# Kernel optimization log

Hardware: AMD Instinct MI355X
Metric: run time of the kernel (lower is better)

The kernel has to match this reference:

```python
import jax, jax.numpy as jnp
import numpy as np

L = 2048      # seq_len
E = 2048      # hidden_dim
H = 16        # num_heads
D = E // H    # head_dim


def setup_inputs() -> dict:
    key = jax.random.key(0)
    ks = jax.random.split(key, 6)
    x = jax.random.normal(ks[0], (L, E), dtype=jnp.float32)
    bias_matrix = jax.random.normal(ks[1], (L, L), dtype=jnp.float32) * 0.1
    # nn.MultiheadAttention params: packed in_proj [3E, E] + bias [3E], out_proj [E, E] + bias [E]
    in_proj_weight = jax.random.normal(ks[2], (3 * E, E), dtype=jnp.float32) * 0.02
    in_proj_bias = jax.random.normal(ks[3], (3 * E,), dtype=jnp.float32) * 0.02
    out_proj_weight = jax.random.normal(ks[4], (E, E), dtype=jnp.float32) * 0.02
    out_proj_bias = jax.random.normal(ks[5], (E,), dtype=jnp.float32) * 0.02
    return {
        "x": x,
        "bias_matrix": bias_matrix,
        "in_proj_weight": in_proj_weight,
        "in_proj_bias": in_proj_bias,
        "out_proj_weight": out_proj_weight,
        "out_proj_bias": out_proj_bias,
    }


def reference(x, bias_matrix, in_proj_weight, in_proj_bias, out_proj_weight, out_proj_bias):
    # Packed QKV projection (torch Linear convention: y = x @ W.T + b)
    qkv = x @ in_proj_weight.T + in_proj_bias            # [L, 3E]
    q, k, v = jnp.split(qkv, 3, axis=-1)                 # each [L, E]
    q = q.reshape(L, H, D)
    k = k.reshape(L, H, D)
    v = v.reshape(L, H, D)
    scale = 1.0 / jnp.sqrt(jnp.asarray(D, dtype=x.dtype))
    # scores: [H, L, L]; bias_matrix broadcast over heads (torch 2D attn_mask semantics)
    scores = jnp.einsum("lhd,mhd->hlm", q * scale, k) + bias_matrix[None, :, :]
    attn = jax.nn.softmax(scores, axis=-1)
    ctx = jnp.einsum("hlm,mhd->lhd", attn, v).reshape(L, E)
    out = ctx @ out_proj_weight.T + out_proj_bias        # [L, E]
    return out
```

## Files before the change

kernel.cpp:

```cpp
#include <hip/hip_runtime.h>
#include <math.h>

#define L_SEQ 2048
#define E_DIM 2048
#define H_NUM 16
#define D_HEAD 128

typedef __attribute__((ext_vector_type(8))) _Float16 half8;
typedef __attribute__((ext_vector_type(4))) _Float16 half4;
typedef __attribute__((ext_vector_type(4))) float floatx4;

static __device__ __forceinline__ void gload16(const void* g, void* lds) {
  __builtin_amdgcn_global_load_lds(
      (const __attribute__((address_space(1))) void*)g,
      (__attribute__((address_space(3))) void*)lds, 16, 0, 0);
}

__global__ __launch_bounds__(256)
void cvt3_f32_f16(const float* __restrict__ a, _Float16* __restrict__ oa, int na,
                  const float* __restrict__ b, _Float16* __restrict__ ob, int nb,
                  const float* __restrict__ c, _Float16* __restrict__ oc, int nc) {
  int i = (blockIdx.x * 256 + threadIdx.x) * 8;
  const float* src;
  _Float16* dst;
  if (i < na) {
    src = a + i; dst = oa + i;
  } else if (i < na + nb) {
    src = b + (i - na); dst = ob + (i - na);
  } else if (i < na + nb + nc) {
    src = c + (i - na - nb); dst = oc + (i - na - nb);
  } else {
    return;
  }
  float4 p = *(const float4*)src;
  float4 q = *(const float4*)(src + 4);
  half8 h = {(_Float16)p.x, (_Float16)p.y, (_Float16)p.z, (_Float16)p.w,
             (_Float16)q.x, (_Float16)q.y, (_Float16)q.z, (_Float16)q.w};
  *(half8*)dst = h;
}

template <int TM, int TN, int WR, int WC, int EPI>
__global__ __launch_bounds__(256)
void gemm_mfma(const _Float16* __restrict__ A, const _Float16* __restrict__ B,
               const float* __restrict__ bias, float* __restrict__ C,
               _Float16* __restrict__ qk, _Float16* __restrict__ vt,
               int M, int N, int K) {
  constexpr int RT = TM / (16 * WR);
  constexpr int CT = TN / (16 * WC);
  constexpr int ACH = TM / 8;
  constexpr int NCH = (TM + TN) / 32;

  __shared__ _Float16 As[2][TM * 64];
  __shared__ _Float16 Bs[2][TN * 64];

  const int tid = threadIdx.x;
  const int wave = tid >> 6, lane = tid & 63;
  const int l15 = lane & 15, quad = lane >> 4;
  const int wr = wave / WC, wc = wave % WC;
  const int row0 = blockIdx.y * TM, col0 = blockIdx.x * TN;

  const int srow = lane >> 3;
  const int gc = (lane & 7) ^ srow;

  auto stage = [&](int buf, int k0) {
#pragma unroll
    for (int c = 0; c < NCH; ++c) {
      int chunk = wave * NCH + c;
      if (chunk < ACH) {
        int row = chunk * 8 + srow;
        gload16((const char*)(A + (size_t)(row0 + row) * K + k0) + gc * 16,
                (char*)&As[buf][0] + chunk * 1024);
      } else {
        int bch = chunk - ACH;
        int row = bch * 8 + srow;
        gload16((const char*)(B + (size_t)(col0 + row) * K + k0) + gc * 16,
                (char*)&Bs[buf][0] + bch * 1024);
      }
    }
  };

  floatx4 acc[RT][CT];
#pragma unroll
  for (int i = 0; i < RT; ++i)
#pragma unroll
    for (int j = 0; j < CT; ++j) acc[i][j] = (floatx4){0.f, 0.f, 0.f, 0.f};

  const int niter = K / 64;
  stage(0, 0);

  for (int it = 0; it < niter; ++it) {
    const int cur = it & 1;
    __syncthreads();
    if (it + 1 < niter) stage(cur ^ 1, (it + 1) * 64);

#pragma unroll
    for (int ks = 0; ks < 2; ++ks) {
      half8 af[RT], bf[CT];
#pragma unroll
      for (int t = 0; t < RT; ++t) {
        int r = wr * (16 * RT) + t * 16 + l15;
        af[t] = *(const half8*)&As[cur][r * 64 + (((ks * 4 + quad) ^ (r & 7)) * 8)];
      }
#pragma unroll
      for (int t = 0; t < CT; ++t) {
        int r = wc * (16 * CT) + t * 16 + l15;
        bf[t] = *(const half8*)&Bs[cur][r * 64 + (((ks * 4 + quad) ^ (r & 7)) * 8)];
      }
#pragma unroll
      for (int tr = 0; tr < RT; ++tr)
#pragma unroll
        for (int tc = 0; tc < CT; ++tc)
          acc[tr][tc] = __builtin_amdgcn_mfma_f32_16x16x32_f16(
              af[tr], bf[tc], acc[tr][tc], 0, 0, 0);
    }
  }

  const int crow = row0 + wr * (16 * RT);
  const int ccol = col0 + wc * (16 * CT);

  if (EPI == 0) {
#pragma unroll
    for (int tc = 0; tc < CT; ++tc) {
      int col = ccol + tc * 16 + l15;
      float bb = bias[col];
#pragma unroll
      for (int tr = 0; tr < RT; ++tr)
#pragma unroll
        for (int r = 0; r < 4; ++r)
          C[(size_t)(crow + tr * 16 + quad * 4 + r) * N + col] =
              acc[tr][tc][r] + bb;
    }
  } else if (col0 < 2 * E_DIM) {
#pragma unroll
    for (int tc = 0; tc < CT; ++tc) {
      int col = ccol + tc * 16 + l15;
      float bb = bias[col];
#pragma unroll
      for (int tr = 0; tr < RT; ++tr)
#pragma unroll
        for (int r = 0; r < 4; ++r)
          qk[(size_t)(crow + tr * 16 + quad * 4 + r) * (2 * E_DIM) + col] =
              (_Float16)(acc[tr][tc][r] + bb);
    }
  } else {
#pragma unroll
    for (int tc = 0; tc < CT; ++tc) {
      int col = ccol + tc * 16 + l15;
      float bb = bias[col];
      int vrow = col - 2 * E_DIM;
#pragma unroll
      for (int tr = 0; tr < RT; ++tr) {
        int rbase = crow + tr * 16 + quad * 4;
        half4 h = {(_Float16)(acc[tr][tc][0] + bb), (_Float16)(acc[tr][tc][1] + bb),
                   (_Float16)(acc[tr][tc][2] + bb), (_Float16)(acc[tr][tc][3] + bb)};
        *(half4*)&vt[(size_t)vrow * L_SEQ + rbase] = h;
      }
    }
  }
}

__global__ __launch_bounds__(512, 2)
void attn_mfma(const _Float16* __restrict__ qk, const _Float16* __restrict__ vt,
               const float* __restrict__ bias, _Float16* __restrict__ ctx) {
  const int h = blockIdx.x;
  const int q0 = blockIdx.y * 128;
  const int tid = threadIdx.x;
  const int wave = tid >> 6;
  const int lane = tid & 63;
  const int l15 = lane & 15;
  const int quad = lane >> 4;

  __shared__ _Float16 Ks[2][64][136];
  __shared__ _Float16 Vst[2][128][72];
  __shared__ _Float16 Ps[128][72];

  half8 qa[4];
  {
    const _Float16* qp = qk + (size_t)(q0 + wave * 16 + l15) * (2 * E_DIM) +
                         h * D_HEAD + quad * 8;
#pragma unroll
    for (int ks = 0; ks < 4; ++ks) qa[ks] = *(const half8*)(qp + ks * 32);
  }

  float l_i = 0.f;
  floatx4 o[8];
#pragma unroll
  for (int t = 0; t < 8; ++t) o[t] = (floatx4){0.f, 0.f, 0.f, 0.f};

  const float scale = 0.088388347648318447f;

  half8 kreg[2], vreg[2];
  floatx4 bcur[4], bnxt[4];
#pragma unroll
  for (int c = 0; c < 2; ++c) {
    int m = c * 512 + tid;
    kreg[c] = *(const half8*)(qk + (size_t)(m >> 4) * (2 * E_DIM) + E_DIM +
                              h * D_HEAD + (m & 15) * 8);
    vreg[c] = *(const half8*)(vt + (size_t)(h * D_HEAD + (m >> 3)) * L_SEQ +
                              (m & 7) * 8);
  }
#pragma unroll
  for (int t = 0; t < 4; ++t)
    bcur[t] = *(const floatx4*)&bias[(size_t)(q0 + wave * 16 + l15) * L_SEQ +
                                    16 * t + quad * 4];
#pragma unroll
  for (int c = 0; c < 2; ++c) {
    int m = c * 512 + tid;
    *(half8*)&Ks[0][m >> 4][(m & 15) * 8] = kreg[c];
    *(half8*)&Vst[0][m >> 3][(m & 7) * 8] = vreg[c];
  }

#pragma unroll 2
  for (int it = 0; it < 32; ++it) {
    const int cur = it & 1, nxt = cur ^ 1;
    const int kt = it * 64;
    __syncthreads();

    if (it < 31) {
#pragma unroll
      for (int c = 0; c < 2; ++c) {
        int m = c * 512 + tid;
        kreg[c] = *(const half8*)(qk + (size_t)(kt + 64 + (m >> 4)) * (2 * E_DIM) +
                                  E_DIM + h * D_HEAD + (m & 15) * 8);
        vreg[c] = *(const half8*)(vt + (size_t)(h * D_HEAD + (m >> 3)) * L_SEQ +
                                  kt + 64 + (m & 7) * 8);
      }
#pragma unroll
      for (int t = 0; t < 4; ++t)
        bnxt[t] = *(const floatx4*)&bias[(size_t)(q0 + wave * 16 + l15) * L_SEQ +
                                         kt + 64 + 16 * t + quad * 4];
    }

    floatx4 st[4];
#pragma unroll
    for (int t = 0; t < 4; ++t) st[t] = (floatx4){0.f, 0.f, 0.f, 0.f};
#pragma unroll
    for (int ks = 0; ks < 4; ++ks)
#pragma unroll
      for (int t = 0; t < 4; ++t) {
        half8 kf = *(const half8*)&Ks[cur][16 * t + l15][ks * 32 + quad * 8];
        st[t] = __builtin_amdgcn_mfma_f32_16x16x32_f16(kf, qa[ks], st[t], 0, 0, 0);
      }

    {
      float ls = 0.f;
      float ps[4][4];
#pragma unroll
      for (int t = 0; t < 4; ++t)
#pragma unroll
        for (int r = 0; r < 4; ++r) {
          float p = __expf(fmaf(st[t][r], scale, bcur[t][r]));
          ps[t][r] = p;
          ls += p;
        }
      ls += __shfl_xor(ls, 16);
      ls += __shfl_xor(ls, 32);
      l_i += ls;
#pragma unroll
      for (int t = 0; t < 4; ++t) {
        half4 hp = {(_Float16)ps[t][0], (_Float16)ps[t][1],
                    (_Float16)ps[t][2], (_Float16)ps[t][3]};
        *(half4*)&Ps[wave * 16 + l15][16 * t + quad * 4] = hp;
      }
    }

    half8 pa[2];
#pragma unroll
    for (int ks = 0; ks < 2; ++ks)
      pa[ks] = *(const half8*)&Ps[wave * 16 + l15][ks * 32 + quad * 8];
#pragma unroll
    for (int t = 0; t < 8; ++t)
#pragma unroll
      for (int ks = 0; ks < 2; ++ks) {
        half8 vf = *(const half8*)&Vst[cur][16 * t + l15][ks * 32 + quad * 8];
        o[t] = __builtin_amdgcn_mfma_f32_16x16x32_f16(pa[ks], vf, o[t], 0, 0, 0);
      }

    if (it < 31) {
#pragma unroll
      for (int c = 0; c < 2; ++c) {
        int m = c * 512 + tid;
        *(half8*)&Ks[nxt][m >> 4][(m & 15) * 8] = kreg[c];
        *(half8*)&Vst[nxt][m >> 3][(m & 7) * 8] = vreg[c];
      }
#pragma unroll
      for (int t = 0; t < 4; ++t) bcur[t] = bnxt[t];
    }
  }

  float inv[4];
#pragma unroll
  for (int r = 0; r < 4; ++r) inv[r] = 1.f / __shfl(l_i, quad * 4 + r);
#pragma unroll
  for (int t = 0; t < 8; ++t)
#pragma unroll
    for (int r = 0; r < 4; ++r) {
      int row = q0 + wave * 16 + quad * 4 + r;
      ctx[(size_t)row * E_DIM + h * D_HEAD + 16 * t + l15] =
          (_Float16)(o[t][r] * inv[r]);
    }
}

extern "C" void kernel_launch(void* const* d_in, const int* in_sizes, int n_in,
                              void* d_out, int out_size, void* d_ws, size_t ws_size,
                              hipStream_t stream) {
  const float* x          = (const float*)d_in[0];
  const float* bias_mat   = (const float*)d_in[1];
  const float* in_proj_w  = (const float*)d_in[2];
  const float* in_proj_b  = (const float*)d_in[3];
  const float* out_proj_w = (const float*)d_in[4];
  const float* out_proj_b = (const float*)d_in[5];
  float* out = (float*)d_out;

  _Float16* x16 = (_Float16*)d_ws;
  _Float16* w1  = x16 + (size_t)L_SEQ * E_DIM;
  _Float16* w2  = w1 + (size_t)3 * E_DIM * E_DIM;
  _Float16* qk  = w2 + (size_t)E_DIM * E_DIM;
  _Float16* vt  = qk + (size_t)L_SEQ * 2 * E_DIM;
  _Float16* ctx = vt + (size_t)E_DIM * L_SEQ;

  dim3 blk(256);
  const int nx = L_SEQ * E_DIM, nw1 = 3 * E_DIM * E_DIM, nw2 = E_DIM * E_DIM;

  cvt3_f32_f16<<<(nx + nw1 + nw2) / 2048, blk, 0, stream>>>(
      x, x16, nx, in_proj_w, w1, nw1, out_proj_w, w2, nw2);

  gemm_mfma<128, 128, 2, 2, 1><<<dim3(3 * E_DIM / 128, L_SEQ / 128), blk, 0, stream>>>(
      x16, w1, in_proj_b, nullptr, qk, vt, L_SEQ, 3 * E_DIM, E_DIM);

  attn_mfma<<<dim3(H_NUM, L_SEQ / 128), dim3(512), 0, stream>>>(qk, vt, bias_mat,
                                                                ctx);

  gemm_mfma<128, 64, 4, 1, 0><<<dim3(E_DIM / 64, L_SEQ / 128), blk, 0, stream>>>(
      ctx, w2, out_proj_b, out, nullptr, nullptr, L_SEQ, E_DIM, E_DIM);
}
```

Baseline: 279.6 us.

## Restructure attention kernel with split-KV wave pairs, async LDS loads, register-resident P

Waves are paired so that each wave handles 32 query rows against its own 64-key half of a 128-key stage. The two partial outputs and row sums are merged through LDS at the end. K/V tiles are fetched straight into swizzled LDS with global_load_lds, replacing the register round-trip and padding. The P matrix stays in registers and feeds 16x16x16 MFMAs directly, which drops the Ps LDS write and read, and each K fragment is now reused for two Q subtiles. The cost is 128KB of LDS per block and more registers, which may limit occupancy below the 2-block launch bound.

```diff
diff --git a/kernel.cpp b/kernel.cpp
--- a/kernel.cpp
+++ b/kernel.cpp
@@ -169,136 +169,164 @@
   const int lane = tid & 63;
   const int l15 = lane & 15;
   const int quad = lane >> 4;
-
-  __shared__ _Float16 Ks[2][64][136];
-  __shared__ _Float16 Vst[2][128][72];
-  __shared__ _Float16 Ps[128][72];
-
-  half8 qa[4];
-  {
-    const _Float16* qp = qk + (size_t)(q0 + wave * 16 + l15) * (2 * E_DIM) +
-                         h * D_HEAD + quad * 8;
-#pragma unroll
-    for (int ks = 0; ks < 4; ++ks) qa[ks] = *(const half8*)(qp + ks * 32);
-  }
-
-  float l_i = 0.f;
-  floatx4 o[8];
-#pragma unroll
-  for (int t = 0; t < 8; ++t) o[t] = (floatx4){0.f, 0.f, 0.f, 0.f};
+  const int g = wave >> 1;
+  const int p = wave & 1;
+
+  __shared__ __align__(16) char smem[131072];
+  char* const ksmem = smem;
+  char* const vsmem = smem + 65536;
+
+  const int qrow = q0 + g * 32;
+
+  half8 qa[2][4];
+#pragma unroll
+  for (int u = 0; u < 2; ++u) {
+    const _Float16* qp =
+        qk + (size_t)(qrow + u * 16 + l15) * (2 * E_DIM) + h * D_HEAD + quad * 8;
+#pragma unroll
+    for (int ks = 0; ks < 4; ++ks) qa[u][ks] = *(const half8*)(qp + ks * 32);
+  }
+
+  float l_acc[2] = {0.f, 0.f};
+  floatx4 o[2][8];
+#pragma unroll
+  for (int u = 0; u < 2; ++u)
+#pragma unroll
+    for (int t = 0; t < 8; ++t) o[u][t] = (floatx4){0.f, 0.f, 0.f, 0.f};
 
   const float scale = 0.088388347648318447f;
 
-  half8 kreg[2], vreg[2];
-  floatx4 bcur[4], bnxt[4];
-#pragma unroll
-  for (int c = 0; c < 2; ++c) {
-    int m = c * 512 + tid;
-    kreg[c] = *(const half8*)(qk + (size_t)(m >> 4) * (2 * E_DIM) + E_DIM +
-                              h * D_HEAD + (m & 15) * 8);
-    vreg[c] = *(const half8*)(vt + (size_t)(h * D_HEAD + (m >> 3)) * L_SEQ +
-                              (m & 7) * 8);
-  }
-#pragma unroll
-  for (int t = 0; t < 4; ++t)
-    bcur[t] = *(const floatx4*)&bias[(size_t)(q0 + wave * 16 + l15) * L_SEQ +
-                                    16 * t + quad * 4];
-#pragma unroll
-  for (int c = 0; c < 2; ++c) {
-    int m = c * 512 + tid;
-    *(half8*)&Ks[0][m >> 4][(m & 15) * 8] = kreg[c];
-    *(half8*)&Vst[0][m >> 3][(m & 7) * 8] = vreg[c];
-  }
+  auto stage_pair = [&](int kt2, int sb) {
+#pragma unroll
+    for (int c = 0; c < 8; ++c) {
+      int mb = c * 512 + (tid & ~63);
+      int m = mb + (tid & 63);
+      if (mb < 2048) {
+        int sub = mb >> 10;
+        int idx = m & 1023, idx0 = mb & 1023;
+        int row = idx >> 4, cc = idx & 15;
+        gload16(qk + (size_t)(kt2 + sub * 64 + row) * (2 * E_DIM) + E_DIM +
+                    h * D_HEAD + ((cc ^ (row & 7)) * 8),
+                ksmem + (sb + sub) * 16384 + idx0 * 16);
+      } else {
+        int mm = mb - 2048;
+        int sub = mm >> 10;
+        int idx = (m - 2048) & 1023, idx0 = mm & 1023;
+        int row = idx >> 3, cc = idx & 7;
+        gload16(vt + (size_t)(h * D_HEAD + row) * L_SEQ + kt2 + sub * 64 +
+                    ((cc ^ (row & 7)) * 8),
+                vsmem + (sb + sub) * 16384 + idx0 * 16);
+      }
+    }
+  };
+
+  stage_pair(0, 0);
 
 #pragma unroll 2
-  for (int it = 0; it < 32; ++it) {
-    const int cur = it & 1, nxt = cur ^ 1;
-    const int kt = it * 64;
+  for (int s = 0; s < 16; ++s) {
+    const int kt = s * 128 + p * 64;
+    const int slot = (s & 1) * 2 + p;
     __syncthreads();
 
-    if (it < 31) {
-#pragma unroll
-      for (int c = 0; c < 2; ++c) {
-        int m = c * 512 + tid;
-        kreg[c] = *(const half8*)(qk + (size_t)(kt + 64 + (m >> 4)) * (2 * E_DIM) +
-                                  E_DIM + h * D_HEAD + (m & 15) * 8);
-        vreg[c] = *(const half8*)(vt + (size_t)(h * D_HEAD + (m >> 3)) * L_SEQ +
-                                  kt + 64 + (m & 7) * 8);
-      }
-#pragma unroll
-      for (int t = 0; t < 4; ++t)
-        bnxt[t] = *(const floatx4*)&bias[(size_t)(q0 + wave * 16 + l15) * L_SEQ +
-                                         kt + 64 + 16 * t + quad * 4];
-    }
-
-    floatx4 st[4];
-#pragma unroll
-    for (int t = 0; t < 4; ++t) st[t] = (floatx4){0.f, 0.f, 0.f, 0.f};
+    floatx4 bq[2][4];
+#pragma unroll
+    for (int u = 0; u < 2; ++u)
+#pragma unroll
+      for (int t4 = 0; t4 < 4; ++t4)
+        bq[u][t4] = *(const floatx4*)&bias[(size_t)(qrow + u * 16 + l15) * L_SEQ +
+                                           kt + t4 * 16 + quad * 4];
+
+    if (s < 15) stage_pair((s + 1) * 128, ((s + 1) & 1) * 2);
+
+    const char* ksb = ksmem + slot * 16384;
+    floatx4 st[2][4];
+#pragma unroll
+    for (int u = 0; u < 2; ++u)
+#pragma unroll
+      for (int t4 = 0; t4 < 4; ++t4) st[u][t4] = (floatx4){0.f, 0.f, 0.f, 0.f};
 #pragma unroll
     for (int ks = 0; ks < 4; ++ks)
 #pragma unroll
-      for (int t = 0; t < 4; ++t) {
-        half8 kf = *(const half8*)&Ks[cur][16 * t + l15][ks * 32 + quad * 8];
-        st[t] = __builtin_amdgcn_mfma_f32_16x16x32_f16(kf, qa[ks], st[t], 0, 0, 0);
-      }
-
-    {
+      for (int t4 = 0; t4 < 4; ++t4) {
+        int row = t4 * 16 + l15;
+        half8 kf = *(const half8*)(ksb + row * 256 +
+                                   (((4 * ks + quad) ^ (row & 7)) * 16));
+        st[0][t4] = __builtin_amdgcn_mfma_f32_16x16x32_f16(kf, qa[0][ks],
+                                                           st[0][t4], 0, 0, 0);
+        st[1][t4] = __builtin_amdgcn_mfma_f32_16x16x32_f16(kf, qa[1][ks],
+                                                           st[1][t4], 0, 0, 0);
+      }
+
+    half4 hp[2][4];
+#pragma unroll
+    for (int u = 0; u < 2; ++u) {
       float ls = 0.f;
-      float ps[4][4];
-#pragma unroll
-      for (int t = 0; t < 4; ++t)
-#pragma unroll
-        for (int r = 0; r < 4; ++r) {
-          float p = __expf(fmaf(st[t][r], scale, bcur[t][r]));
-          ps[t][r] = p;
-          ls += p;
-        }
+#pragma unroll
+      for (int t4 = 0; t4 < 4; ++t4) {
+        float p0 = __expf(fmaf(st[u][t4][0], scale, bq[u][t4][0]));
+        float p1 = __expf(fmaf(st[u][t4][1], scale, bq[u][t4][1]));
+        float p2 = __expf(fmaf(st[u][t4][2], scale, bq[u][t4][2]));
+        float p3 = __expf(fmaf(st[u][t4][3], scale, bq[u][t4][3]));
+        ls += (p0 + p1) + (p2 + p3);
+        hp[u][t4] = (half4){(_Float16)p0, (_Float16)p1, (_Float16)p2, (_Float16)p3};
+      }
       ls += __shfl_xor(ls, 16);
       ls += __shfl_xor(ls, 32);
-      l_i += ls;
-#pragma unroll
-      for (int t = 0; t < 4; ++t) {
-        half4 hp = {(_Float16)ps[t][0], (_Float16)ps[t][1],
-                    (_Float16)ps[t][2], (_Float16)ps[t][3]};
-        *(half4*)&Ps[wave * 16 + l15][16 * t + quad * 4] = hp;
-      }
-    }
-
-    half8 pa[2];
-#pragma unroll
-    for (int ks = 0; ks < 2; ++ks)
-      pa[ks] = *(const half8*)&Ps[wave * 16 + l15][ks * 32 + quad * 8];
-#pragma unroll
-    for (int t = 0; t < 8; ++t)
-#pragma unroll
-      for (int ks = 0; ks < 2; ++ks) {
-        half8 vf = *(const half8*)&Vst[cur][16 * t + l15][ks * 32 + quad * 8];
-        o[t] = __builtin_amdgcn_mfma_f32_16x16x32_f16(pa[ks], vf, o[t], 0, 0, 0);
-      }
-
-    if (it < 31) {
-#pragma unroll
-      for (int c = 0; c < 2; ++c) {
-        int m = c * 512 + tid;
-        *(half8*)&Ks[nxt][m >> 4][(m & 15) * 8] = kreg[c];
-        *(half8*)&Vst[nxt][m >> 3][(m & 7) * 8] = vreg[c];
-      }
-#pragma unroll
-      for (int t = 0; t < 4; ++t) bcur[t] = bnxt[t];
-    }
-  }
-
-  float inv[4];
-#pragma unroll
-  for (int r = 0; r < 4; ++r) inv[r] = 1.f / __shfl(l_i, quad * 4 + r);
-#pragma unroll
-  for (int t = 0; t < 8; ++t)
-#pragma unroll
-    for (int r = 0; r < 4; ++r) {
-      int row = q0 + wave * 16 + quad * 4 + r;
-      ctx[(size_t)row * E_DIM + h * D_HEAD + 16 * t + l15] =
-          (_Float16)(o[t][r] * inv[r]);
-    }
+      l_acc[u] += ls;
+    }
+
+    const char* vsb = vsmem + slot * 16384;
+#pragma unroll
+    for (int tk = 0; tk < 4; ++tk)
+#pragma unroll
+      for (int td = 0; td < 8; ++td) {
+        int row = td * 16 + l15;
+        half4 vf = *(const half4*)(vsb + row * 128 +
+                                   (((2 * tk + (quad >> 1)) ^ (row & 7)) * 16) +
+                                   (quad & 1) * 8);
+        o[0][td] = __builtin_amdgcn_mfma_f32_16x16x16f16(hp[0][tk], vf,
+                                                         o[0][td], 0, 0, 0);
+        o[1][td] = __builtin_amdgcn_mfma_f32_16x16x16f16(hp[1][tk], vf,
+                                                         o[1][td], 0, 0, 0);
+      }
+  }
+
+  float* obuf = (float*)smem;
+  float* lbuf = (float*)(smem + 73728);
+  __syncthreads();
+  if (p == 1) {
+#pragma unroll
+    for (int u = 0; u < 2; ++u)
+#pragma unroll
+      for (int t = 0; t < 8; ++t)
+        *(floatx4*)&obuf[(size_t)(g * 128 + t * 16 + l15) * 36 + u * 16 + quad * 4] =
+            o[u][t];
+    if (quad == 0) {
+      lbuf[(g * 2 + 0) * 16 + l15] = l_acc[0];
+      lbuf[(g * 2 + 1) * 16 + l15] = l_acc[1];
+    }
+  }
+  __syncthreads();
+  if (p == 0) {
+#pragma unroll
+    for (int u = 0; u < 2; ++u) {
+      float lt = l_acc[u] + lbuf[(g * 2 + u) * 16 + l15];
+      float inv[4];
+#pragma unroll
+      for (int r = 0; r < 4; ++r) inv[r] = 1.f / __shfl(lt, quad * 4 + r);
+#pragma unroll
+      for (int t = 0; t < 8; ++t) {
+        floatx4 part = *(const floatx4*)&obuf[(size_t)(g * 128 + t * 16 + l15) * 36 +
+                                              u * 16 + quad * 4];
+#pragma unroll
+        for (int r = 0; r < 4; ++r) {
+          int rowq = qrow + u * 16 + quad * 4 + r;
+          ctx[(size_t)rowq * E_DIM + h * D_HEAD + t * 16 + l15] =
+              (_Float16)((o[u][t][r] + part[r]) * inv[r]);
+        }
+      }
+    }
+  }
 }
 
 extern "C" void kernel_launch(void* const* d_in, const int* in_sizes, int n_in,
```

Result: no change. 282.7 us (+1.1%).

## Add dedicated 256x256-tile QKV GEMM kernel with deeper LDS pipelining

Applied to the files above, without the earlier changes.

Replaces the generic 128x128 QKV projection GEMM with a specialized kernel using 512 threads, 256x256 output tiles and 128 KB of LDS. K is split into half-tiles staged through a multi-slot buffer with explicit vmcnt waits, so global-to-LDS loads overlap MFMA compute. The larger tile raises arithmetic intensity per LDS byte, at the cost of one block per CU and only 192 blocks, which may leave some CUs idle. The generic GEMM template loses its QKV epilogue and keeps only the fp32 output path.

```diff
diff --git a/kernel.cpp b/kernel.cpp
--- a/kernel.cpp
+++ b/kernel.cpp
@@ -39,11 +39,130 @@
   *(half8*)dst = h;
 }
 
-template <int TM, int TN, int WR, int WC, int EPI>
+__global__ __launch_bounds__(512, 1)
+void gemm_qkv(const _Float16* __restrict__ A, const _Float16* __restrict__ B,
+              const float* __restrict__ bias, _Float16* __restrict__ qk,
+              _Float16* __restrict__ vt) {
+  constexpr int K = E_DIM;
+  __shared__ __align__(16) char smem[131072];
+  char* const Asm = smem;
+  char* const Bsm = smem + 65536;
+
+  const int tid = threadIdx.x;
+  const int wave = tid >> 6, lane = tid & 63;
+  const int l15 = lane & 15, quad = lane >> 4;
+  const int wm = wave >> 2, wn = wave & 3;
+  const int brow = blockIdx.y * 256, bcol = blockIdx.x * 256;
+
+  const _Float16* Ag = A + (size_t)brow * K;
+  const _Float16* Bg = B + (size_t)bcol * K;
+
+  auto stg = [&](char* smbase, const _Float16* gbase, int T, int kh) {
+    char* slot = smbase + ((T & 1) * 2 + kh) * 16384;
+#pragma unroll
+    for (int j = 0; j < 2; ++j) {
+      int mb = j * 512 + (tid & ~63);
+      int m = mb + (tid & 63);
+      int row = m >> 2, c = m & 3;
+      gload16(gbase + (size_t)row * K + T * 64 + kh * 32 + ((c ^ (row & 3)) * 8),
+              slot + mb * 16);
+    }
+  };
+
+  floatx4 acc[8][4];
+#pragma unroll
+  for (int i = 0; i < 8; ++i)
+#pragma unroll
+    for (int j = 0; j < 4; ++j) acc[i][j] = (floatx4){0.f, 0.f, 0.f, 0.f};
+
+  auto compute_phase = [&](int T, int ks) {
+    const char* Ab = Asm + ((T & 1) * 2 + ks) * 16384;
+    const char* Bb = Bsm + ((T & 1) * 2 + ks) * 16384;
+    half8 af[8], bf[4];
+#pragma unroll
+    for (int t = 0; t < 8; ++t)
+      af[t] = *(const half8*)(Ab + (size_t)(wm * 128 + t * 16 + l15) * 64 +
+                              ((quad ^ (l15 & 3)) * 16));
+#pragma unroll
+    for (int t = 0; t < 4; ++t)
+      bf[t] = *(const half8*)(Bb + (size_t)(wn * 64 + t * 16 + l15) * 64 +
+                              ((quad ^ (l15 & 3)) * 16));
+#pragma unroll
+    for (int i = 0; i < 8; ++i)
+#pragma unroll
+      for (int j = 0; j < 4; ++j)
+        acc[i][j] = __builtin_amdgcn_mfma_f32_16x16x32_f16(af[i], bf[j],
+                                                           acc[i][j], 0, 0, 0);
+  };
+
+  stg(Asm, Ag, 0, 0); stg(Bsm, Bg, 0, 0);
+  stg(Asm, Ag, 0, 1); stg(Bsm, Bg, 0, 1);
+  stg(Asm, Ag, 1, 0); stg(Bsm, Bg, 1, 0);
+
+  for (int T = 0; T < 31; ++T) {
+    __builtin_amdgcn_sched_barrier(0);
+    asm volatile("s_waitcnt vmcnt(8) lgkmcnt(0)" ::: "memory");
+    __builtin_amdgcn_s_barrier();
+    __builtin_amdgcn_sched_barrier(0);
+    stg(Asm, Ag, T + 1, 1);
+    stg(Bsm, Bg, T + 1, 1);
+    compute_phase(T, 0);
+    __builtin_amdgcn_sched_barrier(0);
+    asm volatile("s_waitcnt vmcnt(8) lgkmcnt(0)" ::: "memory");
+    __builtin_amdgcn_s_barrier();
+    __builtin_amdgcn_sched_barrier(0);
+    if (T < 30) {
+      stg(Asm, Ag, T + 2, 0);
+      stg(Bsm, Bg, T + 2, 0);
+    }
+    compute_phase(T, 1);
+  }
+  __builtin_amdgcn_sched_barrier(0);
+  asm volatile("s_waitcnt vmcnt(4) lgkmcnt(0)" ::: "memory");
+  __builtin_amdgcn_s_barrier();
+  __builtin_amdgcn_sched_barrier(0);
+  compute_phase(31, 0);
+  __builtin_amdgcn_sched_barrier(0);
+  asm volatile("s_waitcnt vmcnt(0) lgkmcnt(0)" ::: "memory");
+  __builtin_amdgcn_s_barrier();
+  __builtin_amdgcn_sched_barrier(0);
+  compute_phase(31, 1);
+
+  const int crow = brow + wm * 128;
+  const int ccol0 = bcol + wn * 64;
+  if (bcol < 2 * E_DIM) {
+#pragma unroll
+    for (int j = 0; j < 4; ++j) {
+      int col = ccol0 + j * 16 + l15;
+      float bb = bias[col];
+#pragma unroll
+      for (int i = 0; i < 8; ++i)
+#pragma unroll
+        for (int r = 0; r < 4; ++r)
+          qk[(size_t)(crow + i * 16 + quad * 4 + r) * (2 * E_DIM) + col] =
+              (_Float16)(acc[i][j][r] + bb);
+    }
+  } else {
+#pragma unroll
+    for (int j = 0; j < 4; ++j) {
+      int col = ccol0 + j * 16 + l15;
+      float bb = bias[col];
+      int vrow = col - 2 * E_DIM;
+#pragma unroll
+      for (int i = 0; i < 8; ++i) {
+        int rbase = crow + i * 16 + quad * 4;
+        half4 h = {(_Float16)(acc[i][j][0] + bb), (_Float16)(acc[i][j][1] + bb),
+                   (_Float16)(acc[i][j][2] + bb), (_Float16)(acc[i][j][3] + bb)};
+        *(half4*)&vt[(size_t)vrow * L_SEQ + rbase] = h;
+      }
+    }
+  }
+}
+
+template <int TM, int TN, int WR, int WC>
 __global__ __launch_bounds__(256)
 void gemm_mfma(const _Float16* __restrict__ A, const _Float16* __restrict__ B,
                const float* __restrict__ bias, float* __restrict__ C,
-               _Float16* __restrict__ qk, _Float16* __restrict__ vt,
                int M, int N, int K) {
   constexpr int RT = TM / (16 * WR);
   constexpr int CT = TN / (16 * WC);
@@ -118,44 +237,16 @@
   const int crow = row0 + wr * (16 * RT);
   const int ccol = col0 + wc * (16 * CT);
 
-  if (EPI == 0) {
-#pragma unroll
-    for (int tc = 0; tc < CT; ++tc) {
-      int col = ccol + tc * 16 + l15;
-      float bb = bias[col];
-#pragma unroll
-      for (int tr = 0; tr < RT; ++tr)
-#pragma unroll
-        for (int r = 0; r < 4; ++r)
-          C[(size_t)(crow + tr * 16 + quad * 4 + r) * N + col] =
-              acc[tr][tc][r] + bb;
-    }
-  } else if (col0 < 2 * E_DIM) {
-#pragma unroll
-    for (int tc = 0; tc < CT; ++tc) {
-      int col = ccol + tc * 16 + l15;
-      float bb = bias[col];
-#pragma unroll
-      for (int tr = 0; tr < RT; ++tr)
-#pragma unroll
-        for (int r = 0; r < 4; ++r)
-          qk[(size_t)(crow + tr * 16 + quad * 4 + r) * (2 * E_DIM) + col] =
-              (_Float16)(acc[tr][tc][r] + bb);
-    }
-  } else {
-#pragma unroll
-    for (int tc = 0; tc < CT; ++tc) {
-      int col = ccol + tc * 16 + l15;
-      float bb = bias[col];
-      int vrow = col - 2 * E_DIM;
-#pragma unroll
-      for (int tr = 0; tr < RT; ++tr) {
-        int rbase = crow + tr * 16 + quad * 4;
-        half4 h = {(_Float16)(acc[tr][tc][0] + bb), (_Float16)(acc[tr][tc][1] + bb),
-                   (_Float16)(acc[tr][tc][2] + bb), (_Float16)(acc[tr][tc][3] + bb)};
-        *(half4*)&vt[(size_t)vrow * L_SEQ + rbase] = h;
-      }
-    }
+#pragma unroll
+  for (int tc = 0; tc < CT; ++tc) {
+    int col = ccol + tc * 16 + l15;
+    float bb = bias[col];
+#pragma unroll
+    for (int tr = 0; tr < RT; ++tr)
+#pragma unroll
+      for (int r = 0; r < 4; ++r)
+        C[(size_t)(crow + tr * 16 + quad * 4 + r) * N + col] =
+            acc[tr][tc][r] + bb;
   }
 }
 
@@ -325,12 +416,12 @@
   cvt3_f32_f16<<<(nx + nw1 + nw2) / 2048, blk, 0, stream>>>(
       x, x16, nx, in_proj_w, w1, nw1, out_proj_w, w2, nw2);
 
-  gemm_mfma<128, 128, 2, 2, 1><<<dim3(3 * E_DIM / 128, L_SEQ / 128), blk, 0, stream>>>(
-      x16, w1, in_proj_b, nullptr, qk, vt, L_SEQ, 3 * E_DIM, E_DIM);
+  gemm_qkv<<<dim3(3 * E_DIM / 256, L_SEQ / 256), dim3(512), 0, stream>>>(
+      x16, w1, in_proj_b, qk, vt);
 
   attn_mfma<<<dim3(H_NUM, L_SEQ / 128), dim3(512), 0, stream>>>(qk, vt, bias_mat,
                                                                 ctx);
 
-  gemm_mfma<128, 64, 4, 1, 0><<<dim3(E_DIM / 64, L_SEQ / 128), blk, 0, stream>>>(
-      ctx, w2, out_proj_b, out, nullptr, nullptr, L_SEQ, E_DIM, E_DIM);
-}
+  gemm_mfma<128, 64, 4, 1><<<dim3(E_DIM / 64, L_SEQ / 128), blk, 0, stream>>>(
+      ctx, w2, out_proj_b, out, L_SEQ, E_DIM, E_DIM);
+}
```

After: 281.2 us. Within noise of the previous version (+0.6%).
